# Kernel tuning notes

Measured on AMD Instinct MI355X. Metric: run time of the kernel, lower is better.

Reference implementation:

```python
import jax, jax.numpy as jnp
import numpy as np
from jax import lax

G, NPER, K = 64, 1024, 512          # graphs, nodes per graph, kept per graph (ceil(0.5*1024))
N, E = G * NPER, 1_048_576          # total nodes, total edges
F, H, C = 128, 128, 10              # in_feats, hidden_dim, num_classes


def gcn(x, src, dst, ew, W, b, num_nodes):
    """PyG GCNConv: D^{-1/2}(A+I)D^{-1/2} X W + b, with edge weights ew."""
    xw = x @ W                                              # [N, H]
    deg = jax.ops.segment_sum(ew, dst, num_segments=num_nodes) + 1.0  # +1 self loop
    dinv = lax.rsqrt(deg)
    coef = dinv[src] * dinv[dst] * ew                       # [E]
    agg = jax.ops.segment_sum(coef[:, None] * xw[src], dst, num_segments=num_nodes)
    return agg + (dinv * dinv)[:, None] * xw + b            # self-loop term + bias


def setup_inputs() -> dict:
    key = jax.random.key(0)
    ks = jax.random.split(key, 10)
    x = jax.random.normal(ks[0], (N, F), jnp.float32)
    # intra-graph random edges: dst forced into same graph block as src
    src = jax.random.randint(ks[1], (E,), 0, N, dtype=jnp.int32)
    dst = (src // NPER) * NPER + jax.random.randint(ks[2], (E,), 0, NPER, dtype=jnp.int32)
    edge_index = jnp.stack([src, dst])                      # [2, E]
    batch = jnp.repeat(jnp.arange(G, dtype=jnp.int32), NPER)
    W1 = jax.random.normal(ks[3], (F, H), jnp.float32) / np.sqrt(F)
    b1 = jnp.zeros((H,), jnp.float32)
    p = jax.random.normal(ks[4], (H,), jnp.float32) / np.sqrt(H)   # TopKPooling score vector
    W2 = jax.random.normal(ks[5], (H, H), jnp.float32) / np.sqrt(H)
    b2 = jnp.zeros((H,), jnp.float32)
    Wl = jax.random.normal(ks[6], (H, C), jnp.float32) / np.sqrt(H)
    bl = jnp.zeros((C,), jnp.float32)
    return dict(x=x, edge_index=edge_index, batch=batch, W1=W1, b1=b1, p=p, W2=W2, b2=b2, Wl=Wl, bl=bl)


def reference(x, edge_index, batch, W1, b1, p, W2, b2, Wl, bl):
    src, dst = edge_index[0], edge_index[1]
    ew1 = jnp.ones((E,), x.dtype)
    h = jax.nn.relu(gcn(x, src, dst, ew1, W1, b1, N))       # conv1 + relu

    # --- TopKPooling: score = tanh(x.p/||p||), keep top-K per graph, gate x by score ---
    score = jnp.tanh((h @ p) / jnp.linalg.norm(p))          # [N]
    vals, idx = lax.top_k(score.reshape(G, NPER), K)        # per-graph top-k, [G, K]
    perm = (idx + jnp.arange(G, dtype=idx.dtype)[:, None] * NPER).reshape(-1)  # global ids [G*K]
    h2 = h[perm] * vals.reshape(-1, 1)                      # gated kept nodes [G*K, H]

    # edge re-index: keep only edges with both endpoints surviving (mask via weight 0)
    new_id = jnp.full((N,), -1, jnp.int32).at[perm].set(jnp.arange(G * K, dtype=jnp.int32))
    s2, d2 = new_id[src], new_id[dst]
    mask = (s2 >= 0) & (d2 >= 0)
    ew2 = mask.astype(h.dtype)
    s2 = jnp.where(mask, s2, 0)
    d2 = jnp.where(mask, d2, 0)

    h3 = jax.nn.relu(gcn(h2, s2, d2, ew2, W2, b2, G * K))   # conv2 + relu

    pooled = h3.reshape(G, K, H).mean(axis=1)               # global_mean_pool (equal counts)
    return pooled @ Wl + bl                                 # [G, C]
```

## Files before the change

### kernel.cpp

```cpp
#include <hip/hip_runtime.h>

#define NNODES 65536
#define NEDGES 1048576
#define NGRAPH 64
#define NPERG  1024
#define KEEP   512
#define M2     (NGRAPH * KEEP)
#define HD     128
#define NC     10
#define EMAX   20480

#define OW1 0
#define OW2 16384
#define OWL 32768
#define OB1 34048
#define OB2 34176
#define OP  34304
#define OBL 34432
#define NCVT 34448

typedef __attribute__((ext_vector_type(8))) short bf16x8;
typedef __attribute__((ext_vector_type(4))) float f32x4;

__device__ __forceinline__ float bf2f(unsigned short u) {
    return __uint_as_float(((unsigned int)u) << 16);
}
__device__ __forceinline__ unsigned short f2bf(float f) {
    unsigned int u = __float_as_uint(f);
    unsigned int r = (u + 0x7FFFu + ((u >> 16) & 1u)) >> 16;
    return (unsigned short)r;
}

__global__ __launch_bounds__(256) void prep_kernel(
    const void* __restrict__ W1, const void* __restrict__ b1, const void* __restrict__ p,
    const void* __restrict__ W2, const void* __restrict__ b2, const void* __restrict__ Wl,
    const void* __restrict__ bl, int* __restrict__ flag, float* __restrict__ cw,
    float* __restrict__ invnorm, int* __restrict__ new_id, int* __restrict__ ghist,
    int* __restrict__ gcur0, float* __restrict__ pooled,
    unsigned short* __restrict__ w1t, unsigned short* __restrict__ w2t,
    const int* __restrict__ src, int* __restrict__ phist) {
    int bid = blockIdx.x, t = threadIdx.x;
    const unsigned short* w1u = (const unsigned short*)W1;
    int local = 0;
    for (int i = t; i < 512; i += 256) {
        unsigned short u = w1u[2 * i];
        int e = (u >> 7) & 0xFF;
        local += (e >= 100 && e <= 140) ? 1 : 0;
    }
    __shared__ int red[256];
    __shared__ int lh[NGRAPH];
    red[t] = local;
    __syncthreads();
    for (int off = 128; off; off >>= 1) {
        if (t < off) red[t] += red[t + off];
        __syncthreads();
    }
    int fl = (red[0] >= 384) ? 1 : 0;
    if (bid == 0 && t == 0) flag[0] = fl;

    if (bid < 135) {
        int gid = bid * 256 + t;
        if (gid < NCVT) {
            const void* srcp; int idx;
            if (gid < OB1) {
                if (gid < OW2)      { srcp = W1; idx = gid - OW1; }
                else if (gid < OWL) { srcp = W2; idx = gid - OW2; }
                else                { srcp = Wl; idx = gid - OWL; }
            } else {
                if (gid < OB2)      { srcp = b1; idx = gid - OB1; }
                else if (gid < OP)  { srcp = b2; idx = gid - OB2; }
                else if (gid < OBL) { srcp = p;  idx = gid - OP; }
                else                { srcp = bl; idx = gid - OBL; }
            }
            float v;
            if (gid >= OWL && gid < OB1 && idx >= 1280) v = 0.f;
            else if (gid >= OBL && idx >= NC) v = 0.f;
            else if (fl) v = bf2f(((const unsigned short*)srcp)[idx]);
            else v = ((const float*)srcp)[idx];
            cw[gid] = v;
            if (gid < OW2) {
                int k = gid >> 7, n = gid & 127;
                w1t[n * 128 + k] = f2bf(v);
            } else if (gid < OWL) {
                int r = gid - OW2;
                int k = r >> 7, n = r & 127;
                w2t[n * 128 + k] = f2bf(v);
            }
        }
    } else if (bid == 135) {
        __shared__ float s2a[128];
        float pv = 0.f;
        if (t < 128) pv = fl ? bf2f(((const unsigned short*)p)[t]) : ((const float*)p)[t];
        if (t < 128) s2a[t] = pv * pv;
        __syncthreads();
        for (int off = 64; off; off >>= 1) {
            if (t < off) s2a[t] += s2a[t + off];
            __syncthreads();
        }
        if (t == 0) invnorm[0] = 1.0f / sqrtf(s2a[0]);
    } else if (bid < 392) {
        int i = (bid - 136) * 256 + t;
        new_id[i] = -1;
        if (i < NGRAPH) { ghist[i] = 0; gcur0[i] = 0; }
        if (i < NGRAPH * HD) pooled[i] = 0.f;
    } else {
        if (t < NGRAPH) lh[t] = 0;
        __syncthreads();
        int e0 = (bid - 392) * 4096;
        for (int k = 0; k < 16; k++) atomicAdd(&lh[src[e0 + k * 256 + t] >> 10], 1);
        __syncthreads();
        if (t < NGRAPH) phist[(bid - 392) * 64 + t] = lh[t];
    }
}

__global__ __launch_bounds__(256) void binpass_kernel(const int* __restrict__ src,
                                                      const int* __restrict__ dst,
                                                      const int* __restrict__ phist,
                                                      int* __restrict__ ghist,
                                                      int* __restrict__ gcur0,
                                                      unsigned int* __restrict__ elist) {
    __shared__ int gh[NGRAPH];
    __shared__ int gbS[NGRAPH];
    __shared__ int lh[NGRAPH];
    __shared__ int lbase[NGRAPH];
    __shared__ int qsum[4][NGRAPH];
    int tid = threadIdx.x;
    {
        int g = tid & 63, q = tid >> 6;
        int s = 0;
        for (int b = q * 64; b < q * 64 + 64; b++) s += phist[b * 64 + g];
        qsum[q][g] = s;
    }
    __syncthreads();
    if (tid < NGRAPH) {
        gh[tid] = qsum[0][tid] + qsum[1][tid] + qsum[2][tid] + qsum[3][tid];
        lh[tid] = 0;
        if (blockIdx.x == 0) ghist[tid] = gh[tid];
    }
    __syncthreads();
    if (tid == 0) {
        int s = 0;
        for (int i = 0; i < NGRAPH; i++) { gbS[i] = s; s += gh[i]; }
    }
    __syncthreads();
    int e0 = blockIdx.x * 4096;
    int gs[16]; unsigned int pk[16];
    for (int k = 0; k < 16; k++) {
        int e = e0 + k * 256 + tid;
        int s = src[e], d = dst[e];
        gs[k] = s >> 10;
        pk[k] = (unsigned)(s & 1023) | ((unsigned)(d & 1023) << 10);
        atomicAdd(&lh[gs[k]], 1);
    }
    __syncthreads();
    if (tid < NGRAPH) { lbase[tid] = gbS[tid] + atomicAdd(&gcur0[tid], lh[tid]); lh[tid] = 0; }
    __syncthreads();
    for (int k = 0; k < 16; k++) {
        int g = gs[k];
        int pos = lbase[g] + atomicAdd(&lh[g], 1);
        elist[pos] = pk[k];
    }
}

__global__ __launch_bounds__(1024) void g1csr_kernel(
    const unsigned int* __restrict__ elist, const int* __restrict__ ghist,
    unsigned short* __restrict__ csr16, int* __restrict__ node_base,
    int* __restrict__ deg_out, float* __restrict__ dinv_out,
    const void* __restrict__ Araw, const unsigned short* __restrict__ Wtb,
    unsigned int* __restrict__ Cb, const int* __restrict__ flag) {
    __shared__ unsigned short sc[EMAX];
    __shared__ int cnt[NPERG];
    __shared__ int cur[NPERG];
    __shared__ int wsum[16];
    __shared__ int gh[NGRAPH];
    __shared__ int baseS, nS;
    int bid = blockIdx.x, t = threadIdx.x;
    if (bid < NGRAPH) {
        int g = bid;
        cnt[t] = 0;
        if (t < NGRAPH) gh[t] = ghist[t];
        __syncthreads();
        if (t == 0) {
            int s = 0;
            for (int i = 0; i < g; i++) s += gh[i];
            baseS = s; nS = gh[g];
        }
        __syncthreads();
        int base = baseS;
        int n = nS; if (n > EMAX) n = EMAX;
        for (int j = t; j < n; j += 1024) atomicAdd(&cnt[(elist[base + j] >> 10) & 1023], 1);
        __syncthreads();
        int v = cnt[t];
        int lane = t & 63;
        int x = v;
        for (int off = 1; off < 64; off <<= 1) {
            int y = __shfl_up(x, off);
            if (lane >= off) x += y;
        }
        if (lane == 63) wsum[t >> 6] = x;
        __syncthreads();
        if (t < 16) {
            int wv = wsum[t];
            int wx = wv;
            for (int off = 1; off < 16; off <<= 1) {
                int y = __shfl_up(wx, off);
                if (t >= off) wx += y;
            }
            wsum[t] = wx - wv;
        }
        __syncthreads();
        int excl = x - v + wsum[t >> 6];
        cur[t] = excl;
        deg_out[g * NPERG + t] = v;
        dinv_out[g * NPERG + t] = rsqrtf((float)v + 1.0f);
        node_base[g * NPERG + t] = base + excl;
        __syncthreads();
        for (int j = t; j < n; j += 1024) {
            unsigned int pk = elist[base + j];
            int d = (pk >> 10) & 1023;
            int pos = atomicAdd(&cur[d], 1);
            sc[pos] = (unsigned short)(pk & 1023);
        }
        __syncthreads();
        for (int j = t; j < n; j += 1024) csr16[base + j] = sc[j];
        return;
    }
    int row0 = (bid - NGRAPH) * 256;
    int wave = t >> 6, lane = t & 63;
    int r0 = row0 + wave * 16;
    int row = r0 + (lane & 15);
    int ko = (lane >> 4) * 8;
    f32x4 acc[8];
#pragma unroll
    for (int c = 0; c < 8; c++) acc[c] = (f32x4){0.f, 0.f, 0.f, 0.f};
    bf16x8 afr[4];
    if (flag[0]) {
        const unsigned short* arow = (const unsigned short*)Araw + (size_t)row * HD + ko;
#pragma unroll
        for (int kk = 0; kk < 4; kk++) afr[kk] = *(const bf16x8*)(arow + kk * 32);
    } else {
        const float* arow = (const float*)Araw + (size_t)row * HD + ko;
#pragma unroll
        for (int kk = 0; kk < 4; kk++) {
            float4 f0 = *(const float4*)(arow + kk * 32);
            float4 f1 = *(const float4*)(arow + kk * 32 + 4);
            bf16x8 a;
            a[0] = (short)f2bf(f0.x); a[1] = (short)f2bf(f0.y);
            a[2] = (short)f2bf(f0.z); a[3] = (short)f2bf(f0.w);
            a[4] = (short)f2bf(f1.x); a[5] = (short)f2bf(f1.y);
            a[6] = (short)f2bf(f1.z); a[7] = (short)f2bf(f1.w);
            afr[kk] = a;
        }
    }
    const unsigned short* brow = Wtb + (lane & 15) * HD + ko;
#pragma unroll
    for (int kk = 0; kk < 4; kk++) {
#pragma unroll
        for (int c = 0; c < 8; c++) {
            bf16x8 b = *(const bf16x8*)(brow + c * 16 * HD + kk * 32);
            acc[c] = __builtin_amdgcn_mfma_f32_16x16x32_bf16(afr[kk], b, acc[c], 0, 0, 0);
        }
    }
    int orow0 = r0 + (lane >> 4) * 4;
    bool even = !(lane & 1);
#pragma unroll
    for (int c = 0; c < 8; c++) {
#pragma unroll
        for (int j = 0; j < 4; j++) {
            float v = acc[c][j];
            float pt = __shfl_xor(v, 1);
            if (even) {
                unsigned int u = (unsigned int)f2bf(v) | ((unsigned int)f2bf(pt) << 16);
                Cb[(size_t)(orow0 + j) * 64 + ((c * 16 + (lane & 15)) >> 1)] = u;
            }
        }
    }
}

__global__ __launch_bounds__(256) void s1_pull(const unsigned short* __restrict__ csr16,
                                               const int* __restrict__ node_base,
                                               const int* __restrict__ deg,
                                               const float* __restrict__ dinv,
                                               const unsigned int* __restrict__ xwb,
                                               const float* __restrict__ b1,
                                               const float* __restrict__ pvec,
                                               const float* __restrict__ invnorm,
                                               unsigned int* __restrict__ hb,
                                               float* __restrict__ score) {
    int b = blockIdx.x;
    int xcd = b & 7, j = b >> 3;
    int g = (j >> 8) * 8 + xcd;
    int n = g * NPERG + (j & 255) * 4 + (threadIdx.x >> 6);
    int lane = threadIdx.x & 63;
    int gb = g * NPERG;
    int base = node_base[n], cnt = deg[n];
    int e = 0; float ds = 0.f;
    if (lane < cnt) {
        e = csr16[base + lane];
        ds = dinv[gb + e];
    }
    float a0 = 0.f, a1 = 0.f;
    int klim = cnt < 64 ? cnt : 64;
    int k = 0;
    for (; k + 7 < klim; k += 8) {
        int s0 = __shfl(e, k),     s1 = __shfl(e, k + 1);
        int s2 = __shfl(e, k + 2), s3 = __shfl(e, k + 3);
        int s4 = __shfl(e, k + 4), s5 = __shfl(e, k + 5);
        int s6 = __shfl(e, k + 6), s7 = __shfl(e, k + 7);
        float d0 = __shfl(ds, k),     d1 = __shfl(ds, k + 1);
        float d2 = __shfl(ds, k + 2), d3 = __shfl(ds, k + 3);
        float d4 = __shfl(ds, k + 4), d5 = __shfl(ds, k + 5);
        float d6 = __shfl(ds, k + 6), d7 = __shfl(ds, k + 7);
        unsigned int u0 = xwb[(size_t)(gb + s0) * 64 + lane];
        unsigned int u1 = xwb[(size_t)(gb + s1) * 64 + lane];
        unsigned int u2 = xwb[(size_t)(gb + s2) * 64 + lane];
        unsigned int u3 = xwb[(size_t)(gb + s3) * 64 + lane];
        unsigned int u4 = xwb[(size_t)(gb + s4) * 64 + lane];
        unsigned int u5 = xwb[(size_t)(gb + s5) * 64 + lane];
        unsigned int u6 = xwb[(size_t)(gb + s6) * 64 + lane];
        unsigned int u7 = xwb[(size_t)(gb + s7) * 64 + lane];
        a0 += d0 * __uint_as_float(u0 << 16); a1 += d0 * __uint_as_float(u0 & 0xFFFF0000u);
        a0 += d1 * __uint_as_float(u1 << 16); a1 += d1 * __uint_as_float(u1 & 0xFFFF0000u);
        a0 += d2 * __uint_as_float(u2 << 16); a1 += d2 * __uint_as_float(u2 & 0xFFFF0000u);
        a0 += d3 * __uint_as_float(u3 << 16); a1 += d3 * __uint_as_float(u3 & 0xFFFF0000u);
        a0 += d4 * __uint_as_float(u4 << 16); a1 += d4 * __uint_as_float(u4 & 0xFFFF0000u);
        a0 += d5 * __uint_as_float(u5 << 16); a1 += d5 * __uint_as_float(u5 & 0xFFFF0000u);
        a0 += d6 * __uint_as_float(u6 << 16); a1 += d6 * __uint_as_float(u6 & 0xFFFF0000u);
        a0 += d7 * __uint_as_float(u7 << 16); a1 += d7 * __uint_as_float(u7 & 0xFFFF0000u);
    }
    for (; k + 3 < klim; k += 4) {
        int s0 = __shfl(e, k), s1 = __shfl(e, k + 1);
        int s2 = __shfl(e, k + 2), s3 = __shfl(e, k + 3);
        float d0 = __shfl(ds, k), d1 = __shfl(ds, k + 1);
        float d2 = __shfl(ds, k + 2), d3 = __shfl(ds, k + 3);
        unsigned int u0 = xwb[(size_t)(gb + s0) * 64 + lane];
        unsigned int u1 = xwb[(size_t)(gb + s1) * 64 + lane];
        unsigned int u2 = xwb[(size_t)(gb + s2) * 64 + lane];
        unsigned int u3 = xwb[(size_t)(gb + s3) * 64 + lane];
        a0 += d0 * __uint_as_float(u0 << 16); a1 += d0 * __uint_as_float(u0 & 0xFFFF0000u);
        a0 += d1 * __uint_as_float(u1 << 16); a1 += d1 * __uint_as_float(u1 & 0xFFFF0000u);
        a0 += d2 * __uint_as_float(u2 << 16); a1 += d2 * __uint_as_float(u2 & 0xFFFF0000u);
        a0 += d3 * __uint_as_float(u3 << 16); a1 += d3 * __uint_as_float(u3 & 0xFFFF0000u);
    }
    for (; k < klim; k++) {
        int sk = __shfl(e, k);
        float dk = __shfl(ds, k);
        unsigned int u = xwb[(size_t)(gb + sk) * 64 + lane];
        a0 += dk * __uint_as_float(u << 16); a1 += dk * __uint_as_float(u & 0xFFFF0000u);
    }
    for (; k < cnt; k++) {
        int sk = csr16[base + k];
        float dk = dinv[gb + sk];
        unsigned int u = xwb[(size_t)(gb + sk) * 64 + lane];
        a0 += dk * __uint_as_float(u << 16); a1 += dk * __uint_as_float(u & 0xFFFF0000u);
    }
    float dn = dinv[n];
    float self = dn * dn;
    unsigned int us = xwb[(size_t)n * 64 + lane];
    float2 bb = ((const float2*)b1)[lane];
    float h0 = fmaxf(dn * a0 + self * __uint_as_float(us << 16) + bb.x, 0.f);
    float h1 = fmaxf(dn * a1 + self * __uint_as_float(us & 0xFFFF0000u) + bb.y, 0.f);
    hb[(size_t)n * 64 + lane] = (unsigned int)f2bf(h0) | ((unsigned int)f2bf(h1) << 16);
    float2 pp = ((const float2*)pvec)[lane];
    float sv = h0 * pp.x + h1 * pp.y;
    for (int off = 32; off; off >>= 1) sv += __shfl_down(sv, off);
    if (lane == 0) score[n] = tanhf(sv * invnorm[0]);
}

__global__ __launch_bounds__(1024) void topk_kernel(const float* __restrict__ score,
                                                    float* __restrict__ vals,
                                                    int* __restrict__ perm,
                                                    int* __restrict__ new_id) {
    __shared__ float sv[1024];
    __shared__ int si[1024];
    int g = blockIdx.x, t = threadIdx.x;
    sv[t] = score[g * NPERG + t];
    si[t] = t;
    __syncthreads();
    for (int k = 2; k <= 1024; k <<= 1) {
        for (int j = k >> 1; j > 0; j >>= 1) {
            int l = t ^ j;
            if (l > t) {
                bool desc = ((t & k) == 0);
                float va = sv[t], vb = sv[l];
                int ia = si[t], ib = si[l];
                bool gab = (va > vb) || (va == vb && ia < ib);
                if (gab != desc) { sv[t] = vb; si[t] = ib; sv[l] = va; si[l] = ia; }
            }
            __syncthreads();
        }
    }
    if (t < KEEP) {
        int node = g * NPERG + si[t];
        int slot = g * KEEP + t;
        vals[slot] = sv[t];
        perm[slot] = node;
        new_id[node] = slot;
    }
}

__global__ __launch_bounds__(512) void g2deg_kernel(
    const unsigned int* __restrict__ elist, const int* __restrict__ ghist,
    const int* __restrict__ new_id, float* __restrict__ dinv2,
    const unsigned int* __restrict__ hb, const int* __restrict__ perm,
    const float* __restrict__ vals, const unsigned short* __restrict__ Wtb,
    float* __restrict__ C) {
    __shared__ int d2[KEEP];
    __shared__ int gh[NGRAPH];
    __shared__ int baseS, nS;
    int bid = blockIdx.x, t = threadIdx.x;
    if (bid < NGRAPH) {
        int g = bid;
        if (t < KEEP) d2[t] = 0;
        if (t < NGRAPH) gh[t] = ghist[t];
        __syncthreads();
        if (t == 0) {
            int s = 0;
            for (int i = 0; i < g; i++) s += gh[i];
            baseS = s; nS = gh[g];
        }
        __syncthreads();
        int base = baseS, n = nS;
        int gb = g * NPERG;
        int kb = g * KEEP;
        for (int j = t; j < n; j += 512) {
            unsigned int pk = elist[base + j];
            int s = pk & 1023, d = (pk >> 10) & 1023;
            int ns = new_id[gb + s], nd = new_id[gb + d];
            if (ns >= 0 && nd >= 0) atomicAdd(&d2[nd - kb], 1);
        }
        __syncthreads();
        if (t < KEEP) dinv2[kb + t] = rsqrtf((float)d2[t] + 1.0f);
        return;
    }
    int row0 = (bid - NGRAPH) * 128;
    int wave = t >> 6, lane = t & 63;
    int r0 = row0 + wave * 16;
    int m = r0 + (lane & 15);
    int ko = (lane >> 4) * 8;
    float sc = vals[m];
    const unsigned int* arow = hb + (size_t)perm[m] * 64 + (ko >> 1);
    bf16x8 afr[4];
#pragma unroll
    for (int kk = 0; kk < 4; kk++) {
        uint4 q = *(const uint4*)(arow + kk * 16);
        bf16x8 a;
        a[0] = (short)f2bf(bf2f((unsigned short)q.x) * sc);
        a[1] = (short)f2bf(bf2f((unsigned short)(q.x >> 16)) * sc);
        a[2] = (short)f2bf(bf2f((unsigned short)q.y) * sc);
        a[3] = (short)f2bf(bf2f((unsigned short)(q.y >> 16)) * sc);
        a[4] = (short)f2bf(bf2f((unsigned short)q.z) * sc);
        a[5] = (short)f2bf(bf2f((unsigned short)(q.z >> 16)) * sc);
        a[6] = (short)f2bf(bf2f((unsigned short)q.w) * sc);
        a[7] = (short)f2bf(bf2f((unsigned short)(q.w >> 16)) * sc);
        afr[kk] = a;
    }
    f32x4 acc[8];
#pragma unroll
    for (int c = 0; c < 8; c++) acc[c] = (f32x4){0.f, 0.f, 0.f, 0.f};
    const unsigned short* brow = Wtb + (lane & 15) * HD + ko;
#pragma unroll
    for (int kk = 0; kk < 4; kk++) {
#pragma unroll
        for (int c = 0; c < 8; c++) {
            bf16x8 b = *(const bf16x8*)(brow + c * 16 * HD + kk * 32);
            acc[c] = __builtin_amdgcn_mfma_f32_16x16x32_bf16(afr[kk], b, acc[c], 0, 0, 0);
        }
    }
    int orow0 = r0 + (lane >> 4) * 4;
    bool even = !(lane & 1);
    float2* C2 = (float2*)C;
#pragma unroll
    for (int c = 0; c < 8; c++) {
#pragma unroll
        for (int j = 0; j < 4; j++) {
            float v = acc[c][j];
            float pt = __shfl_xor(v, 1);
            if (even) {
                float2 o = {v, pt};
                C2[(size_t)(orow0 + j) * 64 + ((c * 16 + (lane & 15)) >> 1)] = o;
            }
        }
    }
}

__global__ __launch_bounds__(256) void s2_pull(const unsigned short* __restrict__ csr16,
                                               const int* __restrict__ node_base,
                                               const int* __restrict__ deg,
                                               const int* __restrict__ perm,
                                               const int* __restrict__ new_id,
                                               const float* __restrict__ dinv2,
                                               const float* __restrict__ xw2,
                                               const float* __restrict__ b2,
                                               float* __restrict__ pooled) {
    __shared__ float pr[HD];
    __shared__ int cnk[4][64];
    __shared__ float cds[4][64];
    int tid = threadIdx.x;
    if (tid < HD) pr[tid] = 0.f;
    __syncthreads();
    int b = blockIdx.x;
    int xcd = b & 7, j = b >> 3;
    int g = (j >> 7) * 8 + xcd;
    int wv = tid >> 6;
    int m = g * KEEP + (j & 127) * 4 + wv;
    int lane = tid & 63;
    int node = perm[m];
    int gb = node & ~(NPERG - 1);
    int base = node_base[node], cnt = deg[node];
    int nk = 0; float ds = 0.f;
    if (lane < cnt) {
        int ns = new_id[gb + csr16[base + lane]];
        if (ns >= 0) { nk = ns; ds = dinv2[ns]; }
    }
    unsigned long long msk = __ballot(ds != 0.f);
    int pos = __popcll(msk & ((1ull << lane) - 1ull));
    if (ds != 0.f) { cnk[wv][pos] = nk; cds[wv][pos] = ds; }
    int na = __popcll(msk);
    const float2* xf2 = (const float2*)xw2;
    float a0 = 0.f, a1 = 0.f;
    int k = 0;
    for (; k + 3 < na; k += 4) {
        int s0 = cnk[wv][k], s1 = cnk[wv][k + 1];
        int s2 = cnk[wv][k + 2], s3 = cnk[wv][k + 3];
        float d0 = cds[wv][k], d1 = cds[wv][k + 1];
        float d2 = cds[wv][k + 2], d3 = cds[wv][k + 3];
        float2 v0 = xf2[(size_t)s0 * 64 + lane];
        float2 v1 = xf2[(size_t)s1 * 64 + lane];
        float2 v2 = xf2[(size_t)s2 * 64 + lane];
        float2 v3 = xf2[(size_t)s3 * 64 + lane];
        a0 += d0 * v0.x; a1 += d0 * v0.y;
        a0 += d1 * v1.x; a1 += d1 * v1.y;
        a0 += d2 * v2.x; a1 += d2 * v2.y;
        a0 += d3 * v3.x; a1 += d3 * v3.y;
    }
    for (; k < na; k++) {
        int sk = cnk[wv][k];
        float dk = cds[wv][k];
        float2 v = xf2[(size_t)sk * 64 + lane];
        a0 += dk * v.x; a1 += dk * v.y;
    }
    for (int kk = 64; kk < cnt; kk++) {
        int ns = new_id[gb + csr16[base + kk]];
        if (ns >= 0) {
            float dk = dinv2[ns];
            float2 v = xf2[(size_t)ns * 64 + lane];
            a0 += dk * v.x; a1 += dk * v.y;
        }
    }
    float dn = dinv2[m];
    float self = dn * dn;
    float2 xs = xf2[(size_t)m * 64 + lane];
    float2 bb = ((const float2*)b2)[lane];
    float o0 = fmaxf(dn * a0 + self * xs.x + bb.x, 0.f);
    float o1 = fmaxf(dn * a1 + self * xs.y + bb.y, 0.f);
    atomicAdd(&pr[lane * 2], o0);
    atomicAdd(&pr[lane * 2 + 1], o1);
    __syncthreads();
    if (tid < HD) atomicAdd(&pooled[g * HD + tid], pr[tid]);
}

__global__ __launch_bounds__(128) void outk_kernel(const float* __restrict__ pooled,
                                                   const float* __restrict__ Wl,
                                                   const float* __restrict__ bl,
                                                   void* __restrict__ outv,
                                                   const int* __restrict__ flag) {
    int g = blockIdx.x, t = threadIdx.x;
    __shared__ float sp[HD];
    sp[t] = pooled[g * HD + t] * (1.0f / KEEP);
    __syncthreads();
    if (t < NC) {
        float acc = bl[t];
        for (int hh = 0; hh < HD; hh++) acc += sp[hh] * Wl[hh * NC + t];
        if (flag[0]) ((unsigned short*)outv)[g * NC + t] = f2bf(acc);
        else         ((float*)outv)[g * NC + t] = acc;
    }
}

extern "C" void kernel_launch(void* const* d_in, const int* in_sizes, int n_in,
                              void* d_out, int out_size, void* d_ws, size_t ws_size,
                              hipStream_t stream) {
    const int* ei   = (const int*)d_in[1];
    const int* srcv = ei;
    const int* dstv = ei + NEDGES;

    char* w = (char*)d_ws;
    const size_t MB = 1u << 20;
    const size_t KB = 1024;
    float* dinv1     = (float*)(w + 0);
    float* score     = (float*)(w + 256 * KB);
    float* vals      = (float*)(w + 512 * KB);
    int*   perm      = (int*)(w + 640 * KB);
    int*   new_id    = (int*)(w + 768 * KB);
    int*   deg1      = (int*)(w + 1024 * KB);
    int*   node_base = (int*)(w + 1280 * KB);
    float* dinv2     = (float*)(w + 1536 * KB);
    float* invnorm   = (float*)(w + 1664 * KB);
    int*   flag      = (int*)(w + 1664 * KB + 64);
    int*   ghist     = (int*)(w + 1664 * KB + 1024);
    int*   gcur0     = (int*)(w + 1664 * KB + 2048);
    float* cw        = (float*)(w + 1700 * KB);
    float* pooled    = (float*)(w + 1840 * KB);
    unsigned short* w1t = (unsigned short*)(w + 1880 * KB);
    unsigned short* w2t = (unsigned short*)(w + 1912 * KB);
    int* phist       = (int*)(w + 1944 * KB);
    unsigned int* xw1b = (unsigned int*)(w + 2 * MB);
    float* xw2  = (float*)(w + 18 * MB);
    unsigned int* hb = (unsigned int*)(w + 34 * MB);
    unsigned int* elist    = (unsigned int*)(w + 66 * MB);
    unsigned short* csr16  = (unsigned short*)(w + 70 * MB);

    float* W1f = cw + OW1; float* W2f = cw + OW2; float* Wlf = cw + OWL;
    float* b1f = cw + OB1; float* b2f = cw + OB2; float* pf  = cw + OP;
    float* blf = cw + OBL;
    (void)W1f; (void)W2f;

    prep_kernel<<<648, 256, 0, stream>>>(d_in[3], d_in[4], d_in[5], d_in[6], d_in[7],
                                         d_in[8], d_in[9], flag, cw, invnorm, new_id,
                                         ghist, gcur0, pooled, w1t, w2t, srcv, phist);
    binpass_kernel<<<256, 256, 0, stream>>>(srcv, dstv, phist, ghist, gcur0, elist);
    g1csr_kernel<<<NGRAPH + NNODES / 256, 1024, 0, stream>>>(
        elist, ghist, csr16, node_base, deg1, dinv1, d_in[0], w1t, xw1b, flag);
    s1_pull<<<NNODES / 4, 256, 0, stream>>>(csr16, node_base, deg1, dinv1, xw1b, b1f, pf,
                                            invnorm, hb, score);
    topk_kernel<<<NGRAPH, 1024, 0, stream>>>(score, vals, perm, new_id);
    g2deg_kernel<<<NGRAPH + M2 / 128, 512, 0, stream>>>(
        elist, ghist, new_id, dinv2, hb, perm, vals, w2t, xw2);
    s2_pull<<<M2 / 4, 256, 0, stream>>>(csr16, node_base, deg1, perm, new_id, dinv2,
                                        xw2, b2f, pooled);
    outk_kernel<<<NGRAPH, 128, 0, stream>>>(pooled, Wlf, blf, d_out, flag);

    (void)in_sizes; (void)n_in; (void)out_size; (void)ws_size;
}
```

Baseline: 261.9 us.

## Store conv2 XW in bf16 and use wave shuffles in bitonic top-k

The conv2 feature transform output is now packed as bf16 pairs instead of fp32. This halves the bytes the gather-heavy s2_pull kernel reads per neighbor. Separately, the per-graph bitonic sort keeps each element in registers and does stages with stride below 64 through cross-lane shuffles, so only the larger strides go through shared memory and barriers. The bf16 storage adds rounding error to the second GCN aggregation.

```diff
diff --git a/kernel.cpp b/kernel.cpp
--- a/kernel.cpp
+++ b/kernel.cpp
@@ -374,26 +374,34 @@
     __shared__ float sv[1024];
     __shared__ int si[1024];
     int g = blockIdx.x, t = threadIdx.x;
-    sv[t] = score[g * NPERG + t];
-    si[t] = t;
-    __syncthreads();
+    float v = score[g * NPERG + t];
+    int idx = t;
     for (int k = 2; k <= 1024; k <<= 1) {
         for (int j = k >> 1; j > 0; j >>= 1) {
-            int l = t ^ j;
-            if (l > t) {
-                bool desc = ((t & k) == 0);
-                float va = sv[t], vb = sv[l];
-                int ia = si[t], ib = si[l];
-                bool gab = (va > vb) || (va == vb && ia < ib);
-                if (gab != desc) { sv[t] = vb; si[t] = ib; sv[l] = va; si[l] = ia; }
+            bool desc = ((t & k) == 0);
+            bool up = (t & j) != 0;
+            float vb; int ib;
+            if (j >= 64) {
+                sv[t] = v; si[t] = idx;
+                __syncthreads();
+                vb = sv[t ^ j]; ib = si[t ^ j];
+                bool cmp = (v > vb) || (v == vb && idx < ib);
+                bool keep = up ? (cmp != desc) : (cmp == desc);
+                if (!keep) { v = vb; idx = ib; }
+                __syncthreads();
+            } else {
+                vb = __shfl_xor(v, j);
+                ib = __shfl_xor(idx, j);
+                bool cmp = (v > vb) || (v == vb && idx < ib);
+                bool keep = up ? (cmp != desc) : (cmp == desc);
+                if (!keep) { v = vb; idx = ib; }
             }
-            __syncthreads();
         }
     }
     if (t < KEEP) {
-        int node = g * NPERG + si[t];
+        int node = g * NPERG + idx;
         int slot = g * KEEP + t;
-        vals[slot] = sv[t];
+        vals[slot] = v;
         perm[slot] = node;
         new_id[node] = slot;
     }
@@ -404,7 +412,7 @@
     const int* __restrict__ new_id, float* __restrict__ dinv2,
     const unsigned int* __restrict__ hb, const int* __restrict__ perm,
     const float* __restrict__ vals, const unsigned short* __restrict__ Wtb,
-    float* __restrict__ C) {
+    unsigned int* __restrict__ Cb) {
     __shared__ int d2[KEEP];
     __shared__ int gh[NGRAPH];
     __shared__ int baseS, nS;
@@ -469,7 +477,6 @@
     }
     int orow0 = r0 + (lane >> 4) * 4;
     bool even = !(lane & 1);
-    float2* C2 = (float2*)C;
 #pragma unroll
     for (int c = 0; c < 8; c++) {
 #pragma unroll
@@ -477,8 +484,8 @@
             float v = acc[c][j];
             float pt = __shfl_xor(v, 1);
             if (even) {
-                float2 o = {v, pt};
-                C2[(size_t)(orow0 + j) * 64 + ((c * 16 + (lane & 15)) >> 1)] = o;
+                unsigned int u = (unsigned int)f2bf(v) | ((unsigned int)f2bf(pt) << 16);
+                Cb[(size_t)(orow0 + j) * 64 + ((c * 16 + (lane & 15)) >> 1)] = u;
             }
         }
     }
@@ -490,7 +497,7 @@
                                                const int* __restrict__ perm,
                                                const int* __restrict__ new_id,
                                                const float* __restrict__ dinv2,
-                                               const float* __restrict__ xw2,
+                                               const unsigned int* __restrict__ xwb2,
                                                const float* __restrict__ b2,
                                                float* __restrict__ pooled) {
     __shared__ float pr[HD];
@@ -517,7 +524,6 @@
     int pos = __popcll(msk & ((1ull << lane) - 1ull));
     if (ds != 0.f) { cnk[wv][pos] = nk; cds[wv][pos] = ds; }
     int na = __popcll(msk);
-    const float2* xf2 = (const float2*)xw2;
     float a0 = 0.f, a1 = 0.f;
     int k = 0;
     for (; k + 3 < na; k += 4) {
@@ -525,35 +531,35 @@
         int s2 = cnk[wv][k + 2], s3 = cnk[wv][k + 3];
         float d0 = cds[wv][k], d1 = cds[wv][k + 1];
         float d2 = cds[wv][k + 2], d3 = cds[wv][k + 3];
-        float2 v0 = xf2[(size_t)s0 * 64 + lane];
-        float2 v1 = xf2[(size_t)s1 * 64 + lane];
-        float2 v2 = xf2[(size_t)s2 * 64 + lane];
-        float2 v3 = xf2[(size_t)s3 * 64 + lane];
-        a0 += d0 * v0.x; a1 += d0 * v0.y;
-        a0 += d1 * v1.x; a1 += d1 * v1.y;
-        a0 += d2 * v2.x; a1 += d2 * v2.y;
-        a0 += d3 * v3.x; a1 += d3 * v3.y;
+        unsigned int u0 = xwb2[(size_t)s0 * 64 + lane];
+        unsigned int u1 = xwb2[(size_t)s1 * 64 + lane];
+        unsigned int u2 = xwb2[(size_t)s2 * 64 + lane];
+        unsigned int u3 = xwb2[(size_t)s3 * 64 + lane];
+        a0 += d0 * __uint_as_float(u0 << 16); a1 += d0 * __uint_as_float(u0 & 0xFFFF0000u);
+        a0 += d1 * __uint_as_float(u1 << 16); a1 += d1 * __uint_as_float(u1 & 0xFFFF0000u);
+        a0 += d2 * __uint_as_float(u2 << 16); a1 += d2 * __uint_as_float(u2 & 0xFFFF0000u);
+        a0 += d3 * __uint_as_float(u3 << 16); a1 += d3 * __uint_as_float(u3 & 0xFFFF0000u);
     }
     for (; k < na; k++) {
         int sk = cnk[wv][k];
         float dk = cds[wv][k];
-        float2 v = xf2[(size_t)sk * 64 + lane];
-        a0 += dk * v.x; a1 += dk * v.y;
+        unsigned int u = xwb2[(size_t)sk * 64 + lane];
+        a0 += dk * __uint_as_float(u << 16); a1 += dk * __uint_as_float(u & 0xFFFF0000u);
     }
     for (int kk = 64; kk < cnt; kk++) {
         int ns = new_id[gb + csr16[base + kk]];
         if (ns >= 0) {
             float dk = dinv2[ns];
-            float2 v = xf2[(size_t)ns * 64 + lane];
-            a0 += dk * v.x; a1 += dk * v.y;
+            unsigned int u = xwb2[(size_t)ns * 64 + lane];
+            a0 += dk * __uint_as_float(u << 16); a1 += dk * __uint_as_float(u & 0xFFFF0000u);
         }
     }
     float dn = dinv2[m];
     float self = dn * dn;
-    float2 xs = xf2[(size_t)m * 64 + lane];
+    unsigned int us = xwb2[(size_t)m * 64 + lane];
     float2 bb = ((const float2*)b2)[lane];
-    float o0 = fmaxf(dn * a0 + self * xs.x + bb.x, 0.f);
-    float o1 = fmaxf(dn * a1 + self * xs.y + bb.y, 0.f);
+    float o0 = fmaxf(dn * a0 + self * __uint_as_float(us << 16) + bb.x, 0.f);
+    float o1 = fmaxf(dn * a1 + self * __uint_as_float(us & 0xFFFF0000u) + bb.y, 0.f);
     atomicAdd(&pr[lane * 2], o0);
     atomicAdd(&pr[lane * 2 + 1], o1);
     __syncthreads();
@@ -605,7 +611,7 @@
     unsigned short* w2t = (unsigned short*)(w + 1912 * KB);
     int* phist       = (int*)(w + 1944 * KB);
     unsigned int* xw1b = (unsigned int*)(w + 2 * MB);
-    float* xw2  = (float*)(w + 18 * MB);
+    unsigned int* xw2b = (unsigned int*)(w + 18 * MB);
     unsigned int* hb = (unsigned int*)(w + 34 * MB);
     unsigned int* elist    = (unsigned int*)(w + 66 * MB);
     unsigned short* csr16  = (unsigned short*)(w + 70 * MB);
@@ -625,9 +631,9 @@
                                             invnorm, hb, score);
     topk_kernel<<<NGRAPH, 1024, 0, stream>>>(score, vals, perm, new_id);
     g2deg_kernel<<<NGRAPH + M2 / 128, 512, 0, stream>>>(
-        elist, ghist, new_id, dinv2, hb, perm, vals, w2t, xw2);
+        elist, ghist, new_id, dinv2, hb, perm, vals, w2t, xw2b);
     s2_pull<<<M2 / 4, 256, 0, stream>>>(csr16, node_base, deg1, perm, new_id, dinv2,
-                                        xw2, b2f, pooled);
+                                        xw2b, b2f, pooled);
     outk_kernel<<<NGRAPH, 128, 0, stream>>>(pooled, Wlf, blf, d_out, flag);
 
     (void)in_sizes; (void)n_in; (void)out_size; (void)ws_size;
```

Result: faster. 255.7 us (-2.4%).
